# Optimization experiments

Hardware: AMD Instinct MI355X
Metric: run time of the kernel (lower is better)

The kernel has to match this reference:

```python
import jax, jax.numpy as jnp
import numpy as np

N, E = 2048, 65536
EMBED, H0, H1 = 64, 128, 128
VOCAB = 625  # 5**k with k=4
SLOPE = 0.01  # F.leaky_relu_ default negative slope


def setup_inputs() -> dict:
    key = jax.random.key(0)
    ks = jax.random.split(key, 20)
    f = jax.random.normal
    return {
        "node_ids": jax.random.randint(ks[0], (N,), 0, VOCAB),
        "edge_index": jax.random.randint(ks[1], (2, E), 0, N),
        "edge_attr": jax.random.uniform(ks[2], (E, 1), dtype=jnp.float32),
        "m": (jax.random.uniform(ks[3], (N, N)) > 0.5).astype(jnp.float32),
        "emb": f(ks[4], (VOCAB, EMBED), dtype=jnp.float32) * 0.1,
        "l0_lin1": f(ks[5], (H0, EMBED + 1), dtype=jnp.float32) * 0.1,
        "l0_lin2": f(ks[6], (H0, H0), dtype=jnp.float32) * 0.1,
        "l0_att_l": f(ks[7], (H0,), dtype=jnp.float32) * 0.1,
        "l0_att_r": f(ks[8], (EMBED,), dtype=jnp.float32) * 0.1,
        "l0_bias": f(ks[9], (H0,), dtype=jnp.float32) * 0.1,
        "l1_lin1": f(ks[10], (H1, H0 + 1), dtype=jnp.float32) * 0.1,
        "l1_lin2": f(ks[11], (H1, H1), dtype=jnp.float32) * 0.1,
        "l1_att_l": f(ks[12], (H1,), dtype=jnp.float32) * 0.1,
        "l1_att_r": f(ks[13], (H0,), dtype=jnp.float32) * 0.1,
        "l1_bias": f(ks[14], (H1,), dtype=jnp.float32) * 0.1,
        "W1": f(ks[15], (20, (EMBED + H0 + H1) * 2), dtype=jnp.float32) * 0.1,
        "b1": f(ks[16], (20,), dtype=jnp.float32) * 0.1,
        "W2": f(ks[17], (20,), dtype=jnp.float32) * 0.1,
        "b2": f(ks[18], (1,), dtype=jnp.float32) * 0.1,
    }


def _segment_softmax(alpha, index, n):
    # numerically-stable softmax over edges grouped by destination node
    amax = jax.ops.segment_max(alpha, index, num_segments=n)
    amax = jnp.where(jnp.isfinite(amax), amax, 0.0)
    e = jnp.exp(alpha - amax[index])
    denom = jax.ops.segment_sum(e, index, num_segments=n)
    return e / (denom[index] + 1e-16)


def _gate_conv(x, src, dst, edge_attr, lin1, lin2, att_l, att_r, bias, n):
    # PyG AttentiveFP GATEConv: message = lin2(leaky_relu(lin1([x_j, e]))) * alpha
    h = jax.nn.leaky_relu(jnp.concatenate([x[src], edge_attr], axis=-1) @ lin1.T, SLOPE)  # [E,out]
    alpha = jax.nn.leaky_relu(h @ att_l + x[dst] @ att_r, SLOPE)  # [E]
    alpha = _segment_softmax(alpha, dst, n)
    msg = (h @ lin2.T) * alpha[:, None]
    return jax.ops.segment_sum(msg, dst, num_segments=n) + bias


def reference(node_ids, edge_index, edge_attr, m, emb,
              l0_lin1, l0_lin2, l0_att_l, l0_att_r, l0_bias,
              l1_lin1, l1_lin2, l1_att_l, l1_att_r, l1_bias,
              W1, b1, W2, b2):
    src, dst = edge_index[0], edge_index[1]
    x = emb[node_ids]  # [N, EMBED]
    h1 = jax.nn.relu(_gate_conv(x, src, dst, edge_attr, l0_lin1, l0_lin2, l0_att_l, l0_att_r, l0_bias, N))
    h2 = jax.nn.relu(_gate_conv(h1, src, dst, edge_attr, l1_lin1, l1_lin2, l1_att_l, l1_att_r, l1_bias, N))
    feat = jnp.concatenate([x, h1, h2], axis=-1)  # [N, C], C = EMBED+H0+H1
    C = feat.shape[-1]
    # 1x1 conv over concat([x_i, x_j]) == split linear: out[c,i,j] = W1[c,:C]@feat[i] + W1[c,C:]@feat[j] + b1[c]
    a = feat @ W1[:, :C].T  # [N, 20] row (i) term
    b = feat @ W1[:, C:].T  # [N, 20] col (j) term
    h = jax.nn.relu(a[:, None, :] + b[None, :, :] + b1)  # [N, N, 20]
    logits = (h @ W2 + b2[0]) * m  # [N, N]; mask multiplies logits as in original
    return jax.nn.softmax(logits, axis=1)
```

## Files before the change

kernel.cpp:

```cpp
#include <hip/hip_runtime.h>
#include <math.h>

#define N 2048
#define E 65536
#define EMBED 64
#define H 128
#define NT 20
#define C3 320
#define CAP 96
#define SLOPE 0.01f

__device__ __forceinline__ float leaky(float x) { return x > 0.f ? x : SLOPE * x; }

__device__ __forceinline__ float wave_sum(float v) {
#pragma unroll
    for (int o = 32; o > 0; o >>= 1) v += __shfl_xor(v, o, 64);
    return v;
}

__global__ __launch_bounds__(256) void k_prep(
    const int* __restrict__ ei, const float* __restrict__ eattr,
    int* __restrict__ cursor, int* __restrict__ srcs, float* __restrict__ eas,
    const float* __restrict__ l1_lin1, float* __restrict__ WT1,
    const float* __restrict__ l0_lin2, float* __restrict__ LT0,
    const float* __restrict__ l1_lin2, float* __restrict__ LT1,
    const int* __restrict__ ids, const float* __restrict__ emb,
    const float* __restrict__ l0_lin1,
    float* __restrict__ x, float* __restrict__ A) {
    int b = blockIdx.x;
    int tid = threadIdx.x;
    if (b < 256) {
        int e = b * 256 + tid;
        int d = ei[E + e];
        int pos = atomicAdd(&cursor[d], 1);
        if (pos < CAP) {
            srcs[d * CAP + pos] = ei[e];
            eas[d * CAP + pos] = eattr[e];
        }
    } else if (b < 448) {
        int j = (b - 256) * 256 + tid;
        if (j < 16384) {
            int c = j >> 7, k = j & 127;
            WT1[j] = l1_lin1[k * (H + 1) + c];
        } else if (j < 32768) {
            int jj = j - 16384; int c = jj >> 7, k = jj & 127;
            LT0[jj] = l0_lin2[k * H + c];
        } else {
            int jj = j - 32768; int c = jj >> 7, k = jj & 127;
            LT1[jj] = l1_lin2[k * H + c];
        }
    } else {
        __shared__ float lw[EMBED][130];
        int n0 = (b - 448) * 8;
        for (int j = tid; j < H * (EMBED + 1); j += 256) {
            int k = j / (EMBED + 1), c = j % (EMBED + 1);
            float v = l0_lin1[j];
            if (c < EMBED) lw[c][k] = v;
        }
        for (int idx = tid; idx < 8 * EMBED; idx += 256) {
            int g = idx >> 6, c = idx & 63;
            x[(n0 + g) * EMBED + c] = emb[ids[n0 + g] * EMBED + c];
        }
        __syncthreads();
        int k = tid & 127, half = tid >> 7;
        const float* xr[4];
#pragma unroll
        for (int it = 0; it < 4; it++) {
            int nn = __builtin_amdgcn_readfirstlane(n0 + 2 * it + half);
            xr[it] = emb + (size_t)ids[nn] * EMBED;
        }
        float acc[4] = {0.f, 0.f, 0.f, 0.f};
#pragma unroll 4
        for (int c = 0; c < EMBED; c++) {
            float wt = lw[c][k];
#pragma unroll
            for (int it = 0; it < 4; it++) acc[it] = fmaf(xr[it][c], wt, acc[it]);
        }
#pragma unroll
        for (int it = 0; it < 4; it++) A[(n0 + 2 * it + half) * H + k] = acc[it];
    }
}

__device__ __forceinline__ void gate_wave(
    int dst, int lane, float xr,
    const float* __restrict__ A,
    float w0, float w1, float attl0, float attl1,
    const int* __restrict__ srcs, const float* __restrict__ eas, int cnt,
    float& out0, float& out1) {
    int c0 = 2 * lane;
    int base = dst * CAP;
    float mmax = -INFINITY, s = 0.f, v0 = 0.f, v1 = 0.f;
    for (int i0 = 0; i0 < cnt; i0 += 8) {
        int nb = cnt - i0; if (nb > 8) nb = 8;
        float h0[8], h1[8], p[8];
#pragma unroll
        for (int e = 0; e < 8; e++) {
            float ea = 0.f; float2 av = make_float2(0.f, 0.f);
            if (e < nb) {
                int sn = srcs[base + i0 + e];
                ea = eas[base + i0 + e];
                av = *(const float2*)&A[sn * H + c0];
            }
            h0[e] = leaky(fmaf(w0, ea, av.x));
            h1[e] = leaky(fmaf(w1, ea, av.y));
            p[e] = h0[e] * attl0 + h1[e] * attl1;
        }
#pragma unroll
        for (int o = 32; o > 0; o >>= 1) {
#pragma unroll
            for (int e = 0; e < 8; e++) p[e] += __shfl_xor(p[e], o, 64);
        }
        float alpha[8];
#pragma unroll
        for (int e = 0; e < 8; e++)
            alpha[e] = (e < nb) ? leaky(p[e] + xr) : -INFINITY;
        float mb = alpha[0];
#pragma unroll
        for (int e = 1; e < 8; e++) mb = fmaxf(mb, alpha[e]);
        float mnew = fmaxf(mmax, mb);
        float scale = __expf(mmax - mnew);
        float sw = 0.f, sv0 = 0.f, sv1 = 0.f;
#pragma unroll
        for (int e = 0; e < 8; e++) {
            float we = __expf(alpha[e] - mnew);
            sw += we;
            sv0 = fmaf(we, h0[e], sv0);
            sv1 = fmaf(we, h1[e], sv1);
        }
        s = fmaf(s, scale, sw);
        v0 = fmaf(v0, scale, sv0);
        v1 = fmaf(v1, scale, sv1);
        mmax = mnew;
    }
    float inv = 1.f / (s + 1e-16f);
    out0 = v0 * inv;
    out1 = v1 * inv;
}

__global__ __launch_bounds__(512) void k_g0(
    const float* __restrict__ x, const float* __restrict__ A0,
    const float* __restrict__ l0_lin1,
    const float* __restrict__ att_l, const float* __restrict__ att_r,
    const int* __restrict__ srcs, const float* __restrict__ eas,
    const int* __restrict__ cursor,
    const float* __restrict__ LT0, const float* __restrict__ b0,
    const float* __restrict__ WT1,
    float* __restrict__ h1, float* __restrict__ A1) {
    __shared__ float agg_s[8][H];
    __shared__ float hs[8][H];
    int n0 = blockIdx.x * 8;
    int tid = threadIdx.x;
    int wv = __builtin_amdgcn_readfirstlane(tid >> 6);
    int lane = tid & 63;
    int c0 = 2 * lane;

    int dst = n0 + wv;
    float xr = wave_sum(x[dst * EMBED + lane] * att_r[lane]);
    float attl0 = att_l[c0], attl1 = att_l[c0 + 1];
    float w0 = l0_lin1[c0 * (EMBED + 1) + EMBED];
    float w1 = l0_lin1[(c0 + 1) * (EMBED + 1) + EMBED];
    int cnt = cursor[dst]; if (cnt > CAP) cnt = CAP;

    float o0, o1;
    gate_wave(dst, lane, xr, A0, w0, w1, attl0, attl1, srcs, eas, cnt, o0, o1);
    agg_s[wv][c0] = o0;
    agg_s[wv][c0 + 1] = o1;
    __syncthreads();

    int k = tid & 127, q = tid >> 7;
    float bk = b0[k];
    float acc0 = bk, acc1 = bk;
#pragma unroll 2
    for (int ct = 0; ct < H / 4; ct++) {
        float u0 = LT0[(4 * ct + 0) * H + k];
        float u1 = LT0[(4 * ct + 1) * H + k];
        float u2 = LT0[(4 * ct + 2) * H + k];
        float u3 = LT0[(4 * ct + 3) * H + k];
        float4 f0 = *(const float4*)&agg_s[q][4 * ct];
        float4 f1 = *(const float4*)&agg_s[q + 4][4 * ct];
        acc0 = fmaf(f0.x, u0, acc0); acc0 = fmaf(f0.y, u1, acc0);
        acc0 = fmaf(f0.z, u2, acc0); acc0 = fmaf(f0.w, u3, acc0);
        acc1 = fmaf(f1.x, u0, acc1); acc1 = fmaf(f1.y, u1, acc1);
        acc1 = fmaf(f1.z, u2, acc1); acc1 = fmaf(f1.w, u3, acc1);
    }
    float hv0 = fmaxf(acc0, 0.f), hv1 = fmaxf(acc1, 0.f);
    h1[(n0 + q) * H + k] = hv0;
    h1[(n0 + q + 4) * H + k] = hv1;
    hs[q][k] = hv0;
    hs[q + 4][k] = hv1;
    __syncthreads();

    float a0 = 0.f, a1 = 0.f;
#pragma unroll 2
    for (int ct = 0; ct < H / 4; ct++) {
        float u0 = WT1[(4 * ct + 0) * H + k];
        float u1 = WT1[(4 * ct + 1) * H + k];
        float u2 = WT1[(4 * ct + 2) * H + k];
        float u3 = WT1[(4 * ct + 3) * H + k];
        float4 f0 = *(const float4*)&hs[q][4 * ct];
        float4 f1 = *(const float4*)&hs[q + 4][4 * ct];
        a0 = fmaf(f0.x, u0, a0); a0 = fmaf(f0.y, u1, a0);
        a0 = fmaf(f0.z, u2, a0); a0 = fmaf(f0.w, u3, a0);
        a1 = fmaf(f1.x, u0, a1); a1 = fmaf(f1.y, u1, a1);
        a1 = fmaf(f1.z, u2, a1); a1 = fmaf(f1.w, u3, a1);
    }
    A1[(n0 + q) * H + k] = a0;
    A1[(n0 + q + 4) * H + k] = a1;
}

__global__ __launch_bounds__(512) void k_g1(
    const float* __restrict__ h1g, const float* __restrict__ A1,
    const float* __restrict__ l1_lin1,
    const float* __restrict__ att_l, const float* __restrict__ att_r,
    const int* __restrict__ srcs, const float* __restrict__ eas,
    const int* __restrict__ cursor,
    const float* __restrict__ LT1, const float* __restrict__ bL1,
    const float* __restrict__ x, const float* __restrict__ W1,
    float* __restrict__ aArr, float* __restrict__ bT) {
    __shared__ float agg_s[8][H];
    __shared__ float feat[8][C3];
    int n0 = blockIdx.x * 8;
    int tid = threadIdx.x;
    int wv = __builtin_amdgcn_readfirstlane(tid >> 6);
    int lane = tid & 63;
    int c0 = 2 * lane;

    int dst = n0 + wv;
    float xr = wave_sum(h1g[dst * H + lane] * att_r[lane] +
                        h1g[dst * H + 64 + lane] * att_r[64 + lane]);
    float attl0 = att_l[c0], attl1 = att_l[c0 + 1];
    float w0 = l1_lin1[c0 * (H + 1) + H];
    float w1 = l1_lin1[(c0 + 1) * (H + 1) + H];
    int cnt = cursor[dst]; if (cnt > CAP) cnt = CAP;

    float o0, o1;
    gate_wave(dst, lane, xr, A1, w0, w1, attl0, attl1, srcs, eas, cnt, o0, o1);
    agg_s[wv][c0] = o0;
    agg_s[wv][c0 + 1] = o1;

    for (int idx = tid; idx < 8 * EMBED; idx += 512) {
        int g = idx >> 6, c = idx & 63;
        feat[g][c] = x[(n0 + g) * EMBED + c];
    }
    for (int idx = tid; idx < 8 * H; idx += 512) {
        int g = idx >> 7, c = idx & 127;
        feat[g][EMBED + c] = h1g[(n0 + g) * H + c];
    }
    __syncthreads();

    int k = tid & 127, q = tid >> 7;
    float bk = bL1[k];
    float acc0 = bk, acc1 = bk;
#pragma unroll 2
    for (int ct = 0; ct < H / 4; ct++) {
        float u0 = LT1[(4 * ct + 0) * H + k];
        float u1 = LT1[(4 * ct + 1) * H + k];
        float u2 = LT1[(4 * ct + 2) * H + k];
        float u3 = LT1[(4 * ct + 3) * H + k];
        float4 f0 = *(const float4*)&agg_s[q][4 * ct];
        float4 f1 = *(const float4*)&agg_s[q + 4][4 * ct];
        acc0 = fmaf(f0.x, u0, acc0); acc0 = fmaf(f0.y, u1, acc0);
        acc0 = fmaf(f0.z, u2, acc0); acc0 = fmaf(f0.w, u3, acc0);
        acc1 = fmaf(f1.x, u0, acc1); acc1 = fmaf(f1.y, u1, acc1);
        acc1 = fmaf(f1.z, u2, acc1); acc1 = fmaf(f1.w, u3, acc1);
    }
    feat[q][EMBED + H + k] = fmaxf(acc0, 0.f);
    feat[q + 4][EMBED + H + k] = fmaxf(acc1, 0.f);
    __syncthreads();

    if (tid < 320) {
        int g = tid / 40, u = tid % 40;
        int t = u % 20, side = u / 20;
        const float* wrow = W1 + t * (2 * C3) + side * C3;
        float s = 0.f;
#pragma unroll 4
        for (int ct = 0; ct < C3 / 4; ct++) {
            float4 fv = *(const float4*)&feat[g][4 * ct];
            float4 wv4 = *(const float4*)&wrow[4 * ct];
            s = fmaf(fv.x, wv4.x, s);
            s = fmaf(fv.y, wv4.y, s);
            s = fmaf(fv.z, wv4.z, s);
            s = fmaf(fv.w, wv4.w, s);
        }
        if (side == 0) aArr[(n0 + g) * NT + t] = s;
        else bT[t * N + (n0 + g)] = s;
    }
}

__global__ __launch_bounds__(256) void k_final(const float* __restrict__ aArr,
                                               const float* __restrict__ bT,
                                               const float* __restrict__ b1,
                                               const float* __restrict__ W2,
                                               const float* __restrict__ b2,
                                               const float* __restrict__ mmat,
                                               float* __restrict__ out) {
    __shared__ float red[16];
    int i0 = blockIdx.x * 4;
    int tid = threadIdx.x;
    int lane = tid & 63, wv = tid >> 6;
    float w2r[NT];
#pragma unroll
    for (int t = 0; t < NT; t++) w2r[t] = W2[t];
    float b2v = b2[0];
    float ab[4][NT];
#pragma unroll
    for (int g = 0; g < 4; g++) {
#pragma unroll
        for (int t = 0; t < NT; t++)
            ab[g][t] = aArr[(i0 + g) * NT + t] + b1[t];
    }
    float l[4][8];
    float tmax[4] = {-INFINITY, -INFINITY, -INFINITY, -INFINITY};
#pragma unroll
    for (int it = 0; it < 8; it++) {
        int j = tid + 256 * it;
        float bt[NT];
#pragma unroll
        for (int t = 0; t < NT; t++) bt[t] = bT[t * N + j];
#pragma unroll
        for (int g = 0; g < 4; g++) {
            float s = b2v;
#pragma unroll
            for (int t = 0; t < NT; t++)
                s += fmaxf(ab[g][t] + bt[t], 0.f) * w2r[t];
            s *= mmat[(size_t)(i0 + g) * N + j];
            l[g][it] = s;
            tmax[g] = fmaxf(tmax[g], s);
        }
    }
#pragma unroll
    for (int g = 0; g < 4; g++) {
#pragma unroll
        for (int o = 32; o > 0; o >>= 1)
            tmax[g] = fmaxf(tmax[g], __shfl_xor(tmax[g], o, 64));
    }
    if (lane == 0) {
#pragma unroll
        for (int g = 0; g < 4; g++) red[wv * 4 + g] = tmax[g];
    }
    __syncthreads();
    float mfin[4];
#pragma unroll
    for (int g = 0; g < 4; g++)
        mfin[g] = fmaxf(fmaxf(red[g], red[4 + g]), fmaxf(red[8 + g], red[12 + g]));
    __syncthreads();

    float ts[4] = {0.f, 0.f, 0.f, 0.f};
#pragma unroll
    for (int it = 0; it < 8; it++) {
#pragma unroll
        for (int g = 0; g < 4; g++) {
            float e = __expf(l[g][it] - mfin[g]);
            l[g][it] = e;
            ts[g] += e;
        }
    }
#pragma unroll
    for (int g = 0; g < 4; g++) {
#pragma unroll
        for (int o = 32; o > 0; o >>= 1) ts[g] += __shfl_xor(ts[g], o, 64);
    }
    if (lane == 0) {
#pragma unroll
        for (int g = 0; g < 4; g++) red[wv * 4 + g] = ts[g];
    }
    __syncthreads();
    float inv[4];
#pragma unroll
    for (int g = 0; g < 4; g++)
        inv[g] = 1.f / (red[g] + red[4 + g] + red[8 + g] + red[12 + g]);

#pragma unroll
    for (int it = 0; it < 8; it++) {
        int j = tid + 256 * it;
#pragma unroll
        for (int g = 0; g < 4; g++)
            out[(size_t)(i0 + g) * N + j] = l[g][it] * inv[g];
    }
}

extern "C" void kernel_launch(void* const* d_in, const int* in_sizes, int n_in,
                              void* d_out, int out_size, void* d_ws, size_t ws_size,
                              hipStream_t stream) {
    const int*   node_ids = (const int*)d_in[0];
    const int*   ei       = (const int*)d_in[1];
    const float* eattr    = (const float*)d_in[2];
    const float* mmat     = (const float*)d_in[3];
    const float* emb      = (const float*)d_in[4];
    const float* l0_lin1  = (const float*)d_in[5];
    const float* l0_lin2  = (const float*)d_in[6];
    const float* l0_att_l = (const float*)d_in[7];
    const float* l0_att_r = (const float*)d_in[8];
    const float* l0_bias  = (const float*)d_in[9];
    const float* l1_lin1  = (const float*)d_in[10];
    const float* l1_lin2  = (const float*)d_in[11];
    const float* l1_att_l = (const float*)d_in[12];
    const float* l1_att_r = (const float*)d_in[13];
    const float* l1_bias  = (const float*)d_in[14];
    const float* W1       = (const float*)d_in[15];
    const float* b1       = (const float*)d_in[16];
    const float* W2       = (const float*)d_in[17];
    const float* b2       = (const float*)d_in[18];
    float* out = (float*)d_out;

    char* w = (char*)d_ws;
    auto alloc = [&](size_t bytes) {
        char* p = w;
        w += (bytes + 255) & ~(size_t)255;
        return p;
    };
    int*   cursor = (int*)alloc(N * sizeof(int));
    int*   srcs   = (int*)alloc(N * CAP * sizeof(int));
    float* eas    = (float*)alloc(N * CAP * sizeof(float));
    float* x      = (float*)alloc(N * EMBED * sizeof(float));
    float* A0     = (float*)alloc(N * H * sizeof(float));
    float* A1     = (float*)alloc(N * H * sizeof(float));
    float* h1     = (float*)alloc(N * H * sizeof(float));
    float* aArr   = (float*)alloc(N * NT * sizeof(float));
    float* bT     = (float*)alloc(NT * N * sizeof(float));
    float* WT1    = (float*)alloc(H * H * sizeof(float));
    float* LT0    = (float*)alloc(H * H * sizeof(float));
    float* LT1    = (float*)alloc(H * H * sizeof(float));

    hipMemsetAsync(cursor, 0, N * sizeof(int), stream);

    k_prep<<<704, 256, 0, stream>>>(ei, eattr, cursor, srcs, eas,
                                    l1_lin1, WT1, l0_lin2, LT0, l1_lin2, LT1,
                                    node_ids, emb, l0_lin1, x, A0);
    k_g0<<<N / 8, 512, 0, stream>>>(x, A0, l0_lin1, l0_att_l, l0_att_r,
                                    srcs, eas, cursor, LT0, l0_bias, WT1, h1, A1);
    k_g1<<<N / 8, 512, 0, stream>>>(h1, A1, l1_lin1, l1_att_l, l1_att_r,
                                    srcs, eas, cursor, LT1, l1_bias, x, W1, aArr, bT);
    k_final<<<N / 4, 256, 0, stream>>>(aArr, bT, b1, W2, b2, mmat, out);
}
```

Baseline: 185.8 us.

## Split per-node attention across two waves and shrink blocks for more parallelism

Result: no change. 187.0 us (+0.6%).

```diff
diff --git a/kernel.cpp b/kernel.cpp
--- a/kernel.cpp
+++ b/kernel.cpp
@@ -81,18 +81,18 @@
     }
 }
 
-__device__ __forceinline__ void gate_wave(
+__device__ __forceinline__ void gate_partial(
     int dst, int lane, float xr,
     const float* __restrict__ A,
     float w0, float w1, float attl0, float attl1,
-    const int* __restrict__ srcs, const float* __restrict__ eas, int cnt,
-    float& out0, float& out1) {
+    const int* __restrict__ srcs, const float* __restrict__ eas, int cnt, int i0start,
+    float& m_out, float& s_out, float& v0_out, float& v1_out) {
     int c0 = 2 * lane;
     int base = dst * CAP;
     float mmax = -INFINITY, s = 0.f, v0 = 0.f, v1 = 0.f;
-    for (int i0 = 0; i0 < cnt; i0 += 8) {
+    for (int i0 = i0start; i0 < cnt; i0 += 16) {
         int nb = cnt - i0; if (nb > 8) nb = 8;
-        float h0[8], h1[8], p[8];
+        float h0[8], h1v[8], p[8];
 #pragma unroll
         for (int e = 0; e < 8; e++) {
             float ea = 0.f; float2 av = make_float2(0.f, 0.f);
@@ -102,8 +102,8 @@
                 av = *(const float2*)&A[sn * H + c0];
             }
             h0[e] = leaky(fmaf(w0, ea, av.x));
-            h1[e] = leaky(fmaf(w1, ea, av.y));
-            p[e] = h0[e] * attl0 + h1[e] * attl1;
+            h1v[e] = leaky(fmaf(w1, ea, av.y));
+            p[e] = h0[e] * attl0 + h1v[e] * attl1;
         }
 #pragma unroll
         for (int o = 32; o > 0; o >>= 1) {
@@ -125,19 +125,29 @@
             float we = __expf(alpha[e] - mnew);
             sw += we;
             sv0 = fmaf(we, h0[e], sv0);
-            sv1 = fmaf(we, h1[e], sv1);
+            sv1 = fmaf(we, h1v[e], sv1);
         }
         s = fmaf(s, scale, sw);
         v0 = fmaf(v0, scale, sv0);
         v1 = fmaf(v1, scale, sv1);
         mmax = mnew;
     }
-    float inv = 1.f / (s + 1e-16f);
-    out0 = v0 * inv;
-    out1 = v1 * inv;
-}
-
-__global__ __launch_bounds__(512) void k_g0(
+    m_out = mmax; s_out = s; v0_out = v0; v1_out = v1;
+}
+
+__device__ __forceinline__ void gate_merge(
+    float mA, float sA, float vA0, float vA1,
+    float mB, float sB, float vB0, float vB1,
+    float& o0, float& o1) {
+    float m = fmaxf(mA, mB);
+    if (m == -INFINITY) { o0 = 0.f; o1 = 0.f; return; }
+    float eA = __expf(mA - m), eB = __expf(mB - m);
+    float inv = 1.f / (fmaf(sA, eA, sB * eB) + 1e-16f);
+    o0 = fmaf(vA0, eA, vB0 * eB) * inv;
+    o1 = fmaf(vA1, eA, vB1 * eB) * inv;
+}
+
+__global__ __launch_bounds__(256, 4) void k_g0(
     const float* __restrict__ x, const float* __restrict__ A0,
     const float* __restrict__ l0_lin1,
     const float* __restrict__ att_l, const float* __restrict__ att_r,
@@ -146,30 +156,41 @@
     const float* __restrict__ LT0, const float* __restrict__ b0,
     const float* __restrict__ WT1,
     float* __restrict__ h1, float* __restrict__ A1) {
-    __shared__ float agg_s[8][H];
-    __shared__ float hs[8][H];
-    int n0 = blockIdx.x * 8;
+    __shared__ float vs[4][H];
+    __shared__ float pm[4], ps[4];
+    __shared__ float agg_s[2][H];
+    __shared__ float hs[2][H];
+    int n0 = blockIdx.x * 2;
     int tid = threadIdx.x;
     int wv = __builtin_amdgcn_readfirstlane(tid >> 6);
     int lane = tid & 63;
     int c0 = 2 * lane;
-
-    int dst = n0 + wv;
+    int p = wv >> 1, h = wv & 1;
+    int dst = n0 + p;
+
     float xr = wave_sum(x[dst * EMBED + lane] * att_r[lane]);
     float attl0 = att_l[c0], attl1 = att_l[c0 + 1];
     float w0 = l0_lin1[c0 * (EMBED + 1) + EMBED];
     float w1 = l0_lin1[(c0 + 1) * (EMBED + 1) + EMBED];
     int cnt = cursor[dst]; if (cnt > CAP) cnt = CAP;
 
-    float o0, o1;
-    gate_wave(dst, lane, xr, A0, w0, w1, attl0, attl1, srcs, eas, cnt, o0, o1);
-    agg_s[wv][c0] = o0;
-    agg_s[wv][c0 + 1] = o1;
+    float pm_, ps_, pv0, pv1;
+    gate_partial(dst, lane, xr, A0, w0, w1, attl0, attl1, srcs, eas, cnt, h * 8,
+                 pm_, ps_, pv0, pv1);
+    vs[wv][c0] = pv0; vs[wv][c0 + 1] = pv1;
+    if (lane == 0) { pm[wv] = pm_; ps[wv] = ps_; }
+    __syncthreads();
+    if (h == 0) {
+        float o0, o1;
+        gate_merge(pm_, ps_, pv0, pv1,
+                   pm[wv ^ 1], ps[wv ^ 1], vs[wv ^ 1][c0], vs[wv ^ 1][c0 + 1], o0, o1);
+        agg_s[p][c0] = o0;
+        agg_s[p][c0 + 1] = o1;
+    }
     __syncthreads();
 
     int k = tid & 127, q = tid >> 7;
-    float bk = b0[k];
-    float acc0 = bk, acc1 = bk;
+    float acc0 = b0[k];
 #pragma unroll 2
     for (int ct = 0; ct < H / 4; ct++) {
         float u0 = LT0[(4 * ct + 0) * H + k];
@@ -177,20 +198,15 @@
         float u2 = LT0[(4 * ct + 2) * H + k];
         float u3 = LT0[(4 * ct + 3) * H + k];
         float4 f0 = *(const float4*)&agg_s[q][4 * ct];
-        float4 f1 = *(const float4*)&agg_s[q + 4][4 * ct];
         acc0 = fmaf(f0.x, u0, acc0); acc0 = fmaf(f0.y, u1, acc0);
         acc0 = fmaf(f0.z, u2, acc0); acc0 = fmaf(f0.w, u3, acc0);
-        acc1 = fmaf(f1.x, u0, acc1); acc1 = fmaf(f1.y, u1, acc1);
-        acc1 = fmaf(f1.z, u2, acc1); acc1 = fmaf(f1.w, u3, acc1);
-    }
-    float hv0 = fmaxf(acc0, 0.f), hv1 = fmaxf(acc1, 0.f);
+    }
+    float hv0 = fmaxf(acc0, 0.f);
     h1[(n0 + q) * H + k] = hv0;
-    h1[(n0 + q + 4) * H + k] = hv1;
     hs[q][k] = hv0;
-    hs[q + 4][k] = hv1;
-    __syncthreads();
-
-    float a0 = 0.f, a1 = 0.f;
+    __syncthreads();
+
+    float a0 = 0.f;
 #pragma unroll 2
     for (int ct = 0; ct < H / 4; ct++) {
         float u0 = WT1[(4 * ct + 0) * H + k];
@@ -198,17 +214,13 @@
         float u2 = WT1[(4 * ct + 2) * H + k];
         float u3 = WT1[(4 * ct + 3) * H + k];
         float4 f0 = *(const float4*)&hs[q][4 * ct];
-        float4 f1 = *(const float4*)&hs[q + 4][4 * ct];
         a0 = fmaf(f0.x, u0, a0); a0 = fmaf(f0.y, u1, a0);
         a0 = fmaf(f0.z, u2, a0); a0 = fmaf(f0.w, u3, a0);
-        a1 = fmaf(f1.x, u0, a1); a1 = fmaf(f1.y, u1, a1);
-        a1 = fmaf(f1.z, u2, a1); a1 = fmaf(f1.w, u3, a1);
     }
     A1[(n0 + q) * H + k] = a0;
-    A1[(n0 + q + 4) * H + k] = a1;
-}
-
-__global__ __launch_bounds__(512) void k_g1(
+}
+
+__global__ __launch_bounds__(256, 4) void k_g1(
     const float* __restrict__ h1g, const float* __restrict__ A1,
     const float* __restrict__ l1_lin1,
     const float* __restrict__ att_l, const float* __restrict__ att_r,
@@ -217,15 +229,18 @@
     const float* __restrict__ LT1, const float* __restrict__ bL1,
     const float* __restrict__ x, const float* __restrict__ W1,
     float* __restrict__ aArr, float* __restrict__ bT) {
-    __shared__ float agg_s[8][H];
-    __shared__ float feat[8][C3];
-    int n0 = blockIdx.x * 8;
+    __shared__ float vs[4][H];
+    __shared__ float pm[4], ps[4];
+    __shared__ float agg_s[2][H];
+    __shared__ float feat[2][C3];
+    int n0 = blockIdx.x * 2;
     int tid = threadIdx.x;
     int wv = __builtin_amdgcn_readfirstlane(tid >> 6);
     int lane = tid & 63;
     int c0 = 2 * lane;
-
-    int dst = n0 + wv;
+    int p = wv >> 1, h = wv & 1;
+    int dst = n0 + p;
+
     float xr = wave_sum(h1g[dst * H + lane] * att_r[lane] +
                         h1g[dst * H + 64 + lane] * att_r[64 + lane]);
     float attl0 = att_l[c0], attl1 = att_l[c0 + 1];
@@ -233,24 +248,32 @@
     float w1 = l1_lin1[(c0 + 1) * (H + 1) + H];
     int cnt = cursor[dst]; if (cnt > CAP) cnt = CAP;
 
-    float o0, o1;
-    gate_wave(dst, lane, xr, A1, w0, w1, attl0, attl1, srcs, eas, cnt, o0, o1);
-    agg_s[wv][c0] = o0;
-    agg_s[wv][c0 + 1] = o1;
-
-    for (int idx = tid; idx < 8 * EMBED; idx += 512) {
+    float pm_, ps_, pv0, pv1;
+    gate_partial(dst, lane, xr, A1, w0, w1, attl0, attl1, srcs, eas, cnt, h * 8,
+                 pm_, ps_, pv0, pv1);
+    vs[wv][c0] = pv0; vs[wv][c0 + 1] = pv1;
+    if (lane == 0) { pm[wv] = pm_; ps[wv] = ps_; }
+    __syncthreads();
+    if (h == 0) {
+        float o0, o1;
+        gate_merge(pm_, ps_, pv0, pv1,
+                   pm[wv ^ 1], ps[wv ^ 1], vs[wv ^ 1][c0], vs[wv ^ 1][c0 + 1], o0, o1);
+        agg_s[p][c0] = o0;
+        agg_s[p][c0 + 1] = o1;
+    }
+
+    for (int idx = tid; idx < 2 * EMBED; idx += 256) {
         int g = idx >> 6, c = idx & 63;
         feat[g][c] = x[(n0 + g) * EMBED + c];
     }
-    for (int idx = tid; idx < 8 * H; idx += 512) {
+    for (int idx = tid; idx < 2 * H; idx += 256) {
         int g = idx >> 7, c = idx & 127;
         feat[g][EMBED + c] = h1g[(n0 + g) * H + c];
     }
     __syncthreads();
 
     int k = tid & 127, q = tid >> 7;
-    float bk = bL1[k];
-    float acc0 = bk, acc1 = bk;
+    float acc0 = bL1[k];
 #pragma unroll 2
     for (int ct = 0; ct < H / 4; ct++) {
         float u0 = LT1[(4 * ct + 0) * H + k];
@@ -258,17 +281,13 @@
         float u2 = LT1[(4 * ct + 2) * H + k];
         float u3 = LT1[(4 * ct + 3) * H + k];
         float4 f0 = *(const float4*)&agg_s[q][4 * ct];
-        float4 f1 = *(const float4*)&agg_s[q + 4][4 * ct];
         acc0 = fmaf(f0.x, u0, acc0); acc0 = fmaf(f0.y, u1, acc0);
         acc0 = fmaf(f0.z, u2, acc0); acc0 = fmaf(f0.w, u3, acc0);
-        acc1 = fmaf(f1.x, u0, acc1); acc1 = fmaf(f1.y, u1, acc1);
-        acc1 = fmaf(f1.z, u2, acc1); acc1 = fmaf(f1.w, u3, acc1);
     }
     feat[q][EMBED + H + k] = fmaxf(acc0, 0.f);
-    feat[q + 4][EMBED + H + k] = fmaxf(acc1, 0.f);
-    __syncthreads();
-
-    if (tid < 320) {
+    __syncthreads();
+
+    if (tid < 80) {
         int g = tid / 40, u = tid % 40;
         int t = u % 20, side = u / 20;
         const float* wrow = W1 + t * (2 * C3) + side * C3;
@@ -287,95 +306,111 @@
     }
 }
 
-__global__ __launch_bounds__(256) void k_final(const float* __restrict__ aArr,
-                                               const float* __restrict__ bT,
-                                               const float* __restrict__ b1,
-                                               const float* __restrict__ W2,
-                                               const float* __restrict__ b2,
-                                               const float* __restrict__ mmat,
-                                               float* __restrict__ out) {
-    __shared__ float red[16];
-    int i0 = blockIdx.x * 4;
+__global__ __launch_bounds__(256, 4) void k_final(const float* __restrict__ aArr,
+                                                  const float* __restrict__ bT,
+                                                  const float* __restrict__ b1,
+                                                  const float* __restrict__ W2,
+                                                  const float* __restrict__ b2,
+                                                  const float* __restrict__ mmat,
+                                                  float* __restrict__ out) {
+    __shared__ float red[8];
+    int i0 = blockIdx.x * 2;
     int tid = threadIdx.x;
     int lane = tid & 63, wv = tid >> 6;
     float w2r[NT];
 #pragma unroll
     for (int t = 0; t < NT; t++) w2r[t] = W2[t];
     float b2v = b2[0];
-    float ab[4][NT];
-#pragma unroll
-    for (int g = 0; g < 4; g++) {
+    float ab[2][NT];
+#pragma unroll
+    for (int g = 0; g < 2; g++) {
 #pragma unroll
         for (int t = 0; t < NT; t++)
             ab[g][t] = aArr[(i0 + g) * NT + t] + b1[t];
     }
-    float l[4][8];
-    float tmax[4] = {-INFINITY, -INFINITY, -INFINITY, -INFINITY};
-#pragma unroll
-    for (int it = 0; it < 8; it++) {
-        int j = tid + 256 * it;
-        float bt[NT];
-#pragma unroll
-        for (int t = 0; t < NT; t++) bt[t] = bT[t * N + j];
-#pragma unroll
-        for (int g = 0; g < 4; g++) {
-            float s = b2v;
-#pragma unroll
-            for (int t = 0; t < NT; t++)
-                s += fmaxf(ab[g][t] + bt[t], 0.f) * w2r[t];
-            s *= mmat[(size_t)(i0 + g) * N + j];
-            l[g][it] = s;
-            tmax[g] = fmaxf(tmax[g], s);
-        }
-    }
-#pragma unroll
-    for (int g = 0; g < 4; g++) {
+    float4 l4[2][2];
+    float tmax[2] = {-INFINITY, -INFINITY};
+#pragma unroll
+    for (int it = 0; it < 2; it++) {
+        int j = 4 * tid + 1024 * it;
+        float4 s4[2];
+#pragma unroll
+        for (int g = 0; g < 2; g++) s4[g] = make_float4(b2v, b2v, b2v, b2v);
+#pragma unroll
+        for (int t = 0; t < NT; t++) {
+            float4 bt4 = *(const float4*)&bT[t * N + j];
+#pragma unroll
+            for (int g = 0; g < 2; g++) {
+                float a = ab[g][t], w = w2r[t];
+                s4[g].x = fmaf(fmaxf(a + bt4.x, 0.f), w, s4[g].x);
+                s4[g].y = fmaf(fmaxf(a + bt4.y, 0.f), w, s4[g].y);
+                s4[g].z = fmaf(fmaxf(a + bt4.z, 0.f), w, s4[g].z);
+                s4[g].w = fmaf(fmaxf(a + bt4.w, 0.f), w, s4[g].w);
+            }
+        }
+#pragma unroll
+        for (int g = 0; g < 2; g++) {
+            float4 mm = *(const float4*)&mmat[(size_t)(i0 + g) * N + j];
+            s4[g].x *= mm.x; s4[g].y *= mm.y; s4[g].z *= mm.z; s4[g].w *= mm.w;
+            l4[g][it] = s4[g];
+            tmax[g] = fmaxf(tmax[g], fmaxf(fmaxf(s4[g].x, s4[g].y), fmaxf(s4[g].z, s4[g].w)));
+        }
+    }
+#pragma unroll
+    for (int g = 0; g < 2; g++) {
 #pragma unroll
         for (int o = 32; o > 0; o >>= 1)
             tmax[g] = fmaxf(tmax[g], __shfl_xor(tmax[g], o, 64));
     }
     if (lane == 0) {
 #pragma unroll
-        for (int g = 0; g < 4; g++) red[wv * 4 + g] = tmax[g];
-    }
-    __syncthreads();
-    float mfin[4];
-#pragma unroll
-    for (int g = 0; g < 4; g++)
-        mfin[g] = fmaxf(fmaxf(red[g], red[4 + g]), fmaxf(red[8 + g], red[12 + g]));
-    __syncthreads();
-
-    float ts[4] = {0.f, 0.f, 0.f, 0.f};
-#pragma unroll
-    for (int it = 0; it < 8; it++) {
-#pragma unroll
-        for (int g = 0; g < 4; g++) {
-            float e = __expf(l[g][it] - mfin[g]);
-            l[g][it] = e;
-            ts[g] += e;
-        }
-    }
-#pragma unroll
-    for (int g = 0; g < 4; g++) {
+        for (int g = 0; g < 2; g++) red[wv * 2 + g] = tmax[g];
+    }
+    __syncthreads();
+    float mfin[2];
+#pragma unroll
+    for (int g = 0; g < 2; g++)
+        mfin[g] = fmaxf(fmaxf(red[g], red[2 + g]), fmaxf(red[4 + g], red[6 + g]));
+    __syncthreads();
+
+    float ts[2] = {0.f, 0.f};
+#pragma unroll
+    for (int it = 0; it < 2; it++) {
+#pragma unroll
+        for (int g = 0; g < 2; g++) {
+            float4 v = l4[g][it];
+            v.x = __expf(v.x - mfin[g]);
+            v.y = __expf(v.y - mfin[g]);
+            v.z = __expf(v.z - mfin[g]);
+            v.w = __expf(v.w - mfin[g]);
+            l4[g][it] = v;
+            ts[g] += v.x + v.y + v.z + v.w;
+        }
+    }
+#pragma unroll
+    for (int g = 0; g < 2; g++) {
 #pragma unroll
         for (int o = 32; o > 0; o >>= 1) ts[g] += __shfl_xor(ts[g], o, 64);
     }
     if (lane == 0) {
 #pragma unroll
-        for (int g = 0; g < 4; g++) red[wv * 4 + g] = ts[g];
-    }
-    __syncthreads();
-    float inv[4];
-#pragma unroll
-    for (int g = 0; g < 4; g++)
-        inv[g] = 1.f / (red[g] + red[4 + g] + red[8 + g] + red[12 + g]);
-
-#pragma unroll
-    for (int it = 0; it < 8; it++) {
-        int j = tid + 256 * it;
-#pragma unroll
-        for (int g = 0; g < 4; g++)
-            out[(size_t)(i0 + g) * N + j] = l[g][it] * inv[g];
+        for (int g = 0; g < 2; g++) red[wv * 2 + g] = ts[g];
+    }
+    __syncthreads();
+    float inv[2];
+#pragma unroll
+    for (int g = 0; g < 2; g++)
+        inv[g] = 1.f / (red[g] + red[2 + g] + red[4 + g] + red[6 + g]);
+
+#pragma unroll
+    for (int it = 0; it < 2; it++) {
+        int j = 4 * tid + 1024 * it;
+#pragma unroll
+        for (int g = 0; g < 2; g++) {
+            float4 v = l4[g][it];
+            v.x *= inv[g]; v.y *= inv[g]; v.z *= inv[g]; v.w *= inv[g];
+            *(float4*)&out[(size_t)(i0 + g) * N + j] = v;
+        }
     }
 }
 
@@ -427,9 +462,9 @@
     k_prep<<<704, 256, 0, stream>>>(ei, eattr, cursor, srcs, eas,
                                     l1_lin1, WT1, l0_lin2, LT0, l1_lin2, LT1,
                                     node_ids, emb, l0_lin1, x, A0);
-    k_g0<<<N / 8, 512, 0, stream>>>(x, A0, l0_lin1, l0_att_l, l0_att_r,
+    k_g0<<<N / 2, 256, 0, stream>>>(x, A0, l0_lin1, l0_att_l, l0_att_r,
                                     srcs, eas, cursor, LT0, l0_bias, WT1, h1, A1);
-    k_g1<<<N / 8, 512, 0, stream>>>(h1, A1, l1_lin1, l1_att_l, l1_att_r,
+    k_g1<<<N / 2, 256, 0, stream>>>(h1, A1, l1_lin1, l1_att_l, l1_att_r,
                                     srcs, eas, cursor, LT1, l1_bias, x, W1, aArr, bT);
-    k_final<<<N / 4, 256, 0, stream>>>(aArr, bT, b1, W2, b2, mmat, out);
-}
+    k_final<<<N / 2, 256, 0, stream>>>(aArr, bT, b1, W2, b2, mmat, out);
+}
```
